# Kernel optimization log

Measured on AMD Instinct MI355X. Metric: run time of the kernel, lower is better.

Reference implementation:

```python
import jax, jax.numpy as jnp
import numpy as np

N_NODES = 100000
N_EDGES = 1_600_000
F_IN, HID, N_CLS = 128, 64, 32
NEG_SLOPE = 0.2  # PyG GATv2Conv default


def _segment_softmax(scores, seg, num_segments):
    # numerically stable softmax over edges grouped by destination node
    m = jax.ops.segment_max(scores, seg, num_segments=num_segments)
    ex = jnp.exp(scores - m[seg])
    s = jax.ops.segment_sum(ex, seg, num_segments=num_segments)
    return ex / (s[seg] + 1e-16)


def _gatv2_layer(x, src, dst, Wl, bl, Wr, br, att, bias, num_nodes):
    xl = x @ Wl + bl              # source transform  [N, C]
    xr = x @ Wr + br              # target transform  [N, C]
    # per-edge GATv2 attention logit: a . leaky_relu(xl_j + xr_i)
    e = jax.nn.leaky_relu(xl[src] + xr[dst], NEG_SLOPE) @ att  # [E]
    alpha = _segment_softmax(e, dst, num_nodes)                 # [E]
    out = jax.ops.segment_sum(alpha[:, None] * xl[src], dst, num_segments=num_nodes)
    return out + bias


def _add_self_loops(edge_index, n):
    loops = jnp.arange(n, dtype=edge_index.dtype)
    return jnp.concatenate([edge_index, jnp.stack([loops, loops])], axis=1)


def setup_inputs() -> dict:
    key = jax.random.key(0)
    ks = jax.random.split(key, 8)
    s1 = 1.0 / np.sqrt(F_IN)
    s2 = 1.0 / np.sqrt(HID)
    return {
        "x": jax.random.normal(ks[0], (N_NODES, F_IN), jnp.float32),
        "edge_index": jax.random.randint(ks[1], (2, N_EDGES), 0, N_NODES, jnp.int64),
        "W1l": jax.random.normal(ks[2], (F_IN, HID), jnp.float32) * s1,
        "b1l": jnp.zeros((HID,), jnp.float32),
        "W1r": jax.random.normal(ks[3], (F_IN, HID), jnp.float32) * s1,
        "b1r": jnp.zeros((HID,), jnp.float32),
        "att1": jax.random.normal(ks[4], (HID,), jnp.float32) * s2,
        "bias1": jnp.zeros((HID,), jnp.float32),
        "W2l": jax.random.normal(ks[5], (HID, N_CLS), jnp.float32) * s2,
        "b2l": jnp.zeros((N_CLS,), jnp.float32),
        "W2r": jax.random.normal(ks[6], (HID, N_CLS), jnp.float32) * s2,
        "b2r": jnp.zeros((N_CLS,), jnp.float32),
        "att2": jax.random.normal(ks[7], (N_CLS,), jnp.float32) / np.sqrt(N_CLS),
        "bias2": jnp.zeros((N_CLS,), jnp.float32),
    }


def reference(x, edge_index, W1l, b1l, W1r, b1r, att1, bias1,
              W2l, b2l, W2r, b2r, att2, bias2):
    n = x.shape[0]
    ei = _add_self_loops(edge_index, n)
    src, dst = ei[0], ei[1]
    h = jax.nn.relu(_gatv2_layer(x, src, dst, W1l, b1l, W1r, b1r, att1, bias1, n))
    # F.dropout(training=False) is identity in eval mode
    out = _gatv2_layer(h, src, dst, W2l, b2l, W2r, b2r, att2, bias2, n)
    return out
```

## Files before the change

### kernel.cpp

```cpp
#include <hip/hip_runtime.h>
#include <hip/hip_fp16.h>
#include <math.h>

#define F_IN 128
#define HID 64
#define NCLS 32
#define NEG 0.2f
#define NBKT 128
#define BSH 7
#define BMSK 127
#define CHUNK 4096

using bf8 = __attribute__((ext_vector_type(8))) short;
using f4v = __attribute__((ext_vector_type(4))) float;
typedef _Float16 hv2 __attribute__((ext_vector_type(2)));

__device__ __forceinline__ void f4fma(float4& a, float s, const float4& w) {
    a.x = fmaf(s, w.x, a.x);
    a.y = fmaf(s, w.y, a.y);
    a.z = fmaf(s, w.z, a.z);
    a.w = fmaf(s, w.w, a.w);
}
__device__ __forceinline__ unsigned short f2bf(float f) {
    unsigned u = __float_as_uint(f);
    return (unsigned short)((u + 0x7FFFu + ((u >> 16) & 1u)) >> 16);
}
__device__ __forceinline__ unsigned short f2h(float f) {
    return __half_as_ushort(__float2half(f));
}
__device__ __forceinline__ float h2f(unsigned short u) {
    return __half2float(__ushort_as_half(u));
}
__device__ __forceinline__ unsigned pkaddabs(unsigned a, unsigned b) {
    hv2 r = __builtin_bit_cast(hv2, a) + __builtin_bit_cast(hv2, b);
    return __builtin_bit_cast(unsigned, r) & 0x7FFF7FFFu;
}
__device__ __forceinline__ float fdot2(unsigned a, unsigned b, float c) {
    return __builtin_amdgcn_fdot2(__builtin_bit_cast(hv2, a),
                                  __builtin_bit_cast(hv2, b), c, false);
}
__device__ __forceinline__ float h2lo(unsigned a) {
    return (float)__builtin_bit_cast(hv2, a).x;
}
__device__ __forceinline__ float h2hi(unsigned a) {
    return (float)__builtin_bit_cast(hv2, a).y;
}
template <int CTRL>
__device__ __forceinline__ float dpp_add(float v) {
    int t = __builtin_amdgcn_update_dpp(0, __float_as_int(v), CTRL, 0xf, 0xf, true);
    return v + __int_as_float(t);
}


__global__ __launch_bounds__(256) void bucketHist(const int* __restrict__ ei,
                                                  int Eorig, int Etot,
                                                  int* __restrict__ bucketSize, int BK) {
    __shared__ int h[1024];
    int t = threadIdx.x;
    for (int j = t; j < BK; j += 256) h[j] = 0;
    __syncthreads();
    int base = blockIdx.x * CHUNK;
    int end = base + CHUNK < Etot ? base + CHUNK : Etot;
    for (int i = base + t; i < end; i += 256) {
        int dst = i < Eorig ? ei[Eorig + i] : i - Eorig;
        atomicAdd(&h[dst >> BSH], 1);
    }
    __syncthreads();
    for (int j = t; j < BK; j += 256)
        if (h[j]) atomicAdd(&bucketSize[j], h[j]);
}

__global__ __launch_bounds__(256) void bucketScan(const int* __restrict__ bucketSize,
                                                  int* __restrict__ bucketStart,
                                                  int* __restrict__ bucketCursor,
                                                  int BK, int Etot) {
    __shared__ int sd[256];
    int t = threadIdx.x;
    int v[4]; int ts = 0;
#pragma unroll
    for (int k = 0; k < 4; k++) {
        v[k] = (4 * t + k < BK) ? bucketSize[4 * t + k] : 0;
        ts += v[k];
    }
    sd[t] = ts;
    __syncthreads();
    for (int off = 1; off < 256; off <<= 1) {
        int x = (t >= off) ? sd[t - off] : 0;
        __syncthreads();
        sd[t] += x;
        __syncthreads();
    }
    int excl = sd[t] - ts;
#pragma unroll
    for (int k = 0; k < 4; k++) {
        if (4 * t + k < BK) { bucketStart[4 * t + k] = excl; bucketCursor[4 * t + k] = excl; }
        excl += v[k];
    }
    if (t == 255) bucketStart[BK] = Etot;
}

__global__ __launch_bounds__(256) void bucketScatter(const int* __restrict__ ei,
                                                     int Eorig, int Etot,
                                                     int* __restrict__ bucketCursor,
                                                     int* __restrict__ pairs, int BK) {
    __shared__ int h[1024], lbase[1024], hcur[1024];
    int t = threadIdx.x;
    for (int j = t; j < BK; j += 256) { h[j] = 0; hcur[j] = 0; }
    __syncthreads();
    int base = blockIdx.x * CHUNK;
    int end = base + CHUNK < Etot ? base + CHUNK : Etot;
    for (int i = base + t; i < end; i += 256) {
        int dst = i < Eorig ? ei[Eorig + i] : i - Eorig;
        atomicAdd(&h[dst >> BSH], 1);
    }
    __syncthreads();
    for (int j = t; j < BK; j += 256)
        lbase[j] = h[j] ? atomicAdd(&bucketCursor[j], h[j]) : 0;
    __syncthreads();
    for (int i = base + t; i < end; i += 256) {
        int src, dst;
        if (i < Eorig) { src = ei[i]; dst = ei[Eorig + i]; }
        else           { src = dst = i - Eorig; }
        int b = dst >> BSH;
        int off = atomicAdd(&hcur[b], 1);
        pairs[lbase[b] + off] = (src << BSH) | (dst & BMSK);
    }
}

__global__ __launch_bounds__(256) void bucketCSR(const int* __restrict__ pairs,
                                                 const int* __restrict__ bucketStart,
                                                 int* __restrict__ rowstart,
                                                 int* __restrict__ cnt,
                                                 int* __restrict__ srclist, int N) {
    __shared__ int c[256], cur[256];
    int t = threadIdx.x;
    int b = blockIdx.x;
    int lo = b * NBKT;
    int eb = bucketStart[b], ee = bucketStart[b + 1];
    c[t] = 0;
    __syncthreads();
    for (int i = eb + t; i < ee; i += 256)
        atomicAdd(&c[pairs[i] & BMSK], 1);
    __syncthreads();
    cur[t] = c[t];
    __syncthreads();
    for (int off = 1; off < 256; off <<= 1) {
        int x = (t >= off) ? cur[t - off] : 0;
        __syncthreads();
        cur[t] += x;
        __syncthreads();
    }
    int excl = cur[t] - c[t];
    int node = lo + t;
    if (t < NBKT && node < N) { rowstart[node] = eb + excl; cnt[node] = c[t]; }
    __syncthreads();
    cur[t] = excl;
    __syncthreads();
    for (int i = eb + t; i < ee; i += 256) {
        int v = pairs[i];
        int pos = atomicAdd(&cur[v & BMSK], 1);
        srclist[eb + pos] = v >> BSH;
    }
}

__global__ __launch_bounds__(256) void prepW(const float* __restrict__ Wl,
                                             const float* __restrict__ Wr,
                                             const float* __restrict__ att1,
                                             const float* __restrict__ att2,
                                             uint4* __restrict__ wfrag,
                                             unsigned short* __restrict__ att1h,
                                             unsigned short* __restrict__ att2h) {
    int e = blockIdx.x * 256 + threadIdx.x;
    if (e >= 2048) {
        int i = e - 2048;
        if (i < HID) att1h[i] = f2h(att1[i]);
        else if (i < HID + NCLS) att2h[i - HID] = f2h(att2[i - HID]);
        return;
    }
    int lane = e & 63;
    int kt = (e >> 6) & 3;
    int ct = (e >> 8) & 3;
    int mat = e >> 10;
    const float* W = mat ? Wr : Wl;
    int k0 = kt * 32 + (lane >> 4) * 8;
    int c = ct * 16 + (lane & 15);
    unsigned short h[8];
#pragma unroll
    for (int j = 0; j < 8; j++) h[j] = f2bf(W[(k0 + j) * HID + c]);
    wfrag[e] = *(uint4*)h;
}

__global__ __launch_bounds__(256) void transform1(const float* __restrict__ x,
                                                  const uint4* __restrict__ wfrag,
                                                  const float* __restrict__ bl,
                                                  const float* __restrict__ br,
                                                  const float* __restrict__ att,
                                                  unsigned short* __restrict__ xlh,
                                                  unsigned short* __restrict__ xrh,
                                                  float* __restrict__ sl, int N) {
    __shared__ uint4 sw[2048];
    int t = threadIdx.x;
#pragma unroll
    for (int j = 0; j < 8; j++) sw[t + j * 256] = wfrag[t + j * 256];
    __syncthreads();

    int w = t >> 6, lane = t & 63;
    int nb = blockIdx.x * 64 + w * 16;
    int m = lane & 15, quad = lane >> 4;

    int arow = nb + m; if (arow >= N) arow = N - 1;
    const float* xrow = x + (size_t)arow * F_IN + quad * 8;
    bf8 afr[4];
#pragma unroll
    for (int kt = 0; kt < 4; kt++) {
        float4 lo = *(const float4*)(xrow + kt * 32);
        float4 hi = *(const float4*)(xrow + kt * 32 + 4);
        unsigned short hh[8];
        hh[0] = f2bf(lo.x); hh[1] = f2bf(lo.y); hh[2] = f2bf(lo.z); hh[3] = f2bf(lo.w);
        hh[4] = f2bf(hi.x); hh[5] = f2bf(hi.y); hh[6] = f2bf(hi.z); hh[7] = f2bf(hi.w);
        afr[kt] = *(bf8*)hh;
    }

    float am[4];
#pragma unroll
    for (int ct = 0; ct < 4; ct++) am[ct] = att[ct * 16 + m];
    float slp[4] = {0.f, 0.f, 0.f, 0.f};

#pragma unroll
    for (int mat = 0; mat < 2; mat++) {
        const float* bias = mat ? br : bl;
#pragma unroll
        for (int ct = 0; ct < 4; ct++) {
            f4v acc = {0.f, 0.f, 0.f, 0.f};
#pragma unroll
            for (int kt = 0; kt < 4; kt++) {
                bf8 bfr = *(bf8*)&sw[((mat * 4 + ct) * 4 + kt) * 64 + lane];
                acc = __builtin_amdgcn_mfma_f32_16x16x32_bf16(afr[kt], bfr, acc, 0, 0, 0);
            }
            int ch = ct * 16 + m;
            float bv = bias[ch];
#pragma unroll
            for (int reg = 0; reg < 4; reg++) {
                int node = nb + quad * 4 + reg;
                float o = acc[reg] + bv;
                if (mat) {
                    if (node < N) xrh[(size_t)node * HID + ch] = f2h(o);
                } else {
                    unsigned short hb = f2h(o);
                    slp[reg] = fmaf(am[ct], h2f(hb), slp[reg]);
                    if (node < N) xlh[(size_t)node * HID + ch] = hb;
                }
            }
        }
    }
#pragma unroll
    for (int reg = 0; reg < 4; reg++) {
        slp[reg] = dpp_add<0xB1>(slp[reg]);
        slp[reg] = dpp_add<0x4E>(slp[reg]);
        slp[reg] = dpp_add<0x141>(slp[reg]);
        slp[reg] = dpp_add<0x140>(slp[reg]);
    }
    if (m == 0) {
#pragma unroll
        for (int reg = 0; reg < 4; reg++) {
            int node = nb + quad * 4 + reg;
            if (node < N) sl[node] = 0.6f * slp[reg];
        }
    }
}

__global__ __launch_bounds__(256) void transform2(const float* __restrict__ h,
                                                  const float* __restrict__ Wl,
                                                  const float* __restrict__ bl,
                                                  const float* __restrict__ Wr,
                                                  const float* __restrict__ br,
                                                  const float* __restrict__ att,
                                                  unsigned short* __restrict__ xlh,
                                                  unsigned short* __restrict__ xrh,
                                                  float* __restrict__ sl, int N) {
    __shared__ float sWl[HID * NCLS];
    __shared__ float sWr[HID * NCLS];
    __shared__ float sx[128][68];
    int t = threadIdx.x;
    int nb = blockIdx.x * 128;

#pragma unroll
    for (int j = 0; j < 2; j++) {
        int f = t + j * 256;
        ((float4*)sWl)[f] = ((const float4*)Wl)[f];
        ((float4*)sWr)[f] = ((const float4*)Wr)[f];
    }
    int maxf = (N - nb) * 16;
#pragma unroll
    for (int j = 0; j < 8; j++) {
        int f = t + j * 256;
        int node = f >> 4, kc = f & 15;
        float4 v = {0.f, 0.f, 0.f, 0.f};
        if (f < maxf) v = ((const float4*)(h + (size_t)nb * HID))[f];
        v.x = fmaxf(v.x, 0.f);
        v.y = fmaxf(v.y, 0.f);
        v.z = fmaxf(v.z, 0.f);
        v.w = fmaxf(v.w, 0.f);
        *(float4*)&sx[node][kc * 4] = v;
    }
    __syncthreads();

    int c4 = (t & 7) * 4;
    int slot = t >> 3;
    float4 bl4 = *(const float4*)(bl + c4);
    float4 br4 = *(const float4*)(br + c4);
    float4 at4 = *(const float4*)(att + c4);
    float4 accl[4] = {bl4, bl4, bl4, bl4};
    float4 accr[4] = {br4, br4, br4, br4};

#pragma unroll 4
    for (int k4 = 0; k4 < HID / 4; k4++) {
        int k = k4 * 4;
        float4 wl0 = *(const float4*)&sWl[(k + 0) * NCLS + c4];
        float4 wl1 = *(const float4*)&sWl[(k + 1) * NCLS + c4];
        float4 wl2 = *(const float4*)&sWl[(k + 2) * NCLS + c4];
        float4 wl3 = *(const float4*)&sWl[(k + 3) * NCLS + c4];
        float4 wr0 = *(const float4*)&sWr[(k + 0) * NCLS + c4];
        float4 wr1 = *(const float4*)&sWr[(k + 1) * NCLS + c4];
        float4 wr2 = *(const float4*)&sWr[(k + 2) * NCLS + c4];
        float4 wr3 = *(const float4*)&sWr[(k + 3) * NCLS + c4];
#pragma unroll
        for (int j = 0; j < 4; j++) {
            float4 xv = *(const float4*)&sx[slot + j * 32][k];
            f4fma(accl[j], xv.x, wl0); f4fma(accr[j], xv.x, wr0);
            f4fma(accl[j], xv.y, wl1); f4fma(accr[j], xv.y, wr1);
            f4fma(accl[j], xv.z, wl2); f4fma(accr[j], xv.z, wr2);
            f4fma(accl[j], xv.w, wl3); f4fma(accr[j], xv.w, wr3);
        }
    }
#pragma unroll
    for (int j = 0; j < 4; j++) {
        ushort4 o;
        o.x = f2h(accl[j].x); o.y = f2h(accl[j].y);
        o.z = f2h(accl[j].z); o.w = f2h(accl[j].w);
        ushort4 orr;
        orr.x = f2h(accr[j].x); orr.y = f2h(accr[j].y);
        orr.z = f2h(accr[j].z); orr.w = f2h(accr[j].w);
        float slpj = fmaf(at4.x, h2f(o.x),
                     fmaf(at4.y, h2f(o.y),
                     fmaf(at4.z, h2f(o.z), at4.w * h2f(o.w))));
        slpj = dpp_add<0xB1>(slpj);
        slpj = dpp_add<0x4E>(slpj);
        slpj = dpp_add<0x141>(slpj);
        int g = nb + slot + j * 32;
        if (g < N) {
            *(ushort4*)(xlh + (size_t)g * NCLS + c4) = o;
            *(ushort4*)(xrh + (size_t)g * NCLS + c4) = orr;
            if ((t & 7) == 0) sl[g] = 0.6f * slpj;
        }
    }
}

#define LOADROW(VP, SRC)                                                  \
    {                                                                     \
        const unsigned short* rp = xlh + (unsigned)(SRC) * C + cb0;       \
        if (NH == 4) *(uint4*)(VP) = *(const uint4*)rp;                   \
        else         *(uint2*)(VP) = *(const uint2*)rp;                   \
    }

#define COMPUTE(VP, T, B)                                                 \
    {                                                                     \
        float pa = 0.f;                                                   \
        _Pragma("unroll")                                                 \
        for (int j = 0; j < NH; j++)                                      \
            pa = fdot2(pkaddabs((VP)[j], xrp[j]), atp[j], pa);            \
        pa = dpp_add<0x128>(pa);                                          \
        pa += __shfl_xor(pa, 16, 64);                                     \
        pa += __shfl_xor(pa, 32, 64);                                     \
        float wgt = ((B) * 8 + slot < len) ? __expf(fmaf(0.4f, pa, (T)))  \
                                           : 0.f;                         \
        s += wgt;                                                         \
        _Pragma("unroll")                                                 \
        for (int j = 0; j < NH; j++) {                                    \
            acc[2 * j]     = fmaf(wgt, h2lo((VP)[j]), acc[2 * j]);        \
            acc[2 * j + 1] = fmaf(wgt, h2hi((VP)[j]), acc[2 * j + 1]);    \
        }                                                                 \
    }

template <int C>
__global__ __launch_bounds__(256) void fusedAggG(const unsigned short* __restrict__ xlh,
                                                 const unsigned short* __restrict__ xrh,
                                                 const unsigned short* __restrict__ atth,
                                                 const float* __restrict__ sl,
                                                 const int* __restrict__ rowstart,
                                                 const int* __restrict__ cnt,
                                                 const int* __restrict__ srclist,
                                                 const float* __restrict__ bias,
                                                 float* __restrict__ out, int N) {
    constexpr int CH = C / 8;
    constexpr int NH = CH / 2;
    int wid = threadIdx.x >> 6;
    int lane = threadIdx.x & 63;
    int n = blockIdx.x * 4 + wid;
    if (n >= N) return;

    int slot = lane & 7;
    int pos  = lane >> 3;
    int cb0  = pos * CH;

    unsigned xrp[NH], atp[NH];
    if (NH == 4) {
        *(uint4*)xrp = *(const uint4*)(xrh + (size_t)n * C + cb0);
        *(uint4*)atp = *(const uint4*)(atth + cb0);
    } else {
        *(uint2*)xrp = *(const uint2*)(xrh + (size_t)n * C + cb0);
        *(uint2*)atp = *(const uint2*)(atth + cb0);
    }

    int row = rowstart[n];
    int deg = cnt[n];

    float s = 0.f;
    float acc[CH];
#pragma unroll
    for (int c = 0; c < CH; c++) acc[c] = 0.f;

    for (int cb = 0; cb < deg; cb += 64) {
        int len = deg - cb; if (len > 64) len = 64;
        int len1 = len - 1;
        int li = lane < len ? lane : len1;
        int srcv = srclist[row + cb + li];
        float slv = sl[srcv];
        int nbatch = (len + 7) >> 3;

        float tA = __shfl(slv, slot, 64);
        int srcA = __shfl(srcv, slot, 64);
        unsigned vpA[NH], vpB[NH];
        float tB;
        LOADROW(vpA, srcA)

        int b = 0;
        while (true) {
            bool moreB = (b + 1 < nbatch);
            if (moreB) {
                int e = (b + 1) * 8 + slot;
                tB = __shfl(slv, e, 64);
                int srcB = __shfl(srcv, e, 64);
                LOADROW(vpB, srcB)
            }
            COMPUTE(vpA, tA, b)
            if (!moreB) break;
            bool moreA = (b + 2 < nbatch);
            if (moreA) {
                int e = (b + 2) * 8 + slot;
                tA = __shfl(slv, e, 64);
                int srcA2 = __shfl(srcv, e, 64);
                LOADROW(vpA, srcA2)
            }
            COMPUTE(vpB, tB, b + 1)
            if (!moreA) break;
            b += 2;
        }
    }
#pragma unroll
    for (int c = 0; c < CH; c++) {
        acc[c] = dpp_add<0xB1>(acc[c]);
        acc[c] = dpp_add<0x4E>(acc[c]);
        acc[c] = dpp_add<0x141>(acc[c]);
    }
    s = dpp_add<0xB1>(s);
    s = dpp_add<0x4E>(s);
    s = dpp_add<0x141>(s);

    if (slot == 0) {
        float inv = 1.f / (s + 1e-16f);
        float o8[CH];
        float bi[CH];
        if (NH == 4) {
            *(float4*)&bi[0] = *(const float4*)(bias + cb0);
            *(float4*)&bi[4] = *(const float4*)(bias + cb0 + 4);
        } else {
            *(float4*)&bi[0] = *(const float4*)(bias + cb0);
        }
#pragma unroll
        for (int c = 0; c < CH; c++) o8[c] = fmaf(acc[c], inv, bi[c]);
        if (NH == 4) {
            *(float4*)(out + (size_t)n * C + cb0)     = *(float4*)&o8[0];
            *(float4*)(out + (size_t)n * C + cb0 + 4) = *(float4*)&o8[4];
        } else {
            *(float4*)(out + (size_t)n * C + cb0) = *(float4*)&o8[0];
        }
    }
}

extern "C" void kernel_launch(void* const* d_in, const int* in_sizes, int n_in,
                              void* d_out, int out_size, void* d_ws, size_t ws_size,
                              hipStream_t stream) {
    const float* x     = (const float*)d_in[0];
    const int*   ei    = (const int*)d_in[1];
    const float* W1l   = (const float*)d_in[2];
    const float* b1l   = (const float*)d_in[3];
    const float* W1r   = (const float*)d_in[4];
    const float* b1r   = (const float*)d_in[5];
    const float* att1  = (const float*)d_in[6];
    const float* bias1 = (const float*)d_in[7];
    const float* W2l   = (const float*)d_in[8];
    const float* b2l   = (const float*)d_in[9];
    const float* W2r   = (const float*)d_in[10];
    const float* b2r   = (const float*)d_in[11];
    const float* att2  = (const float*)d_in[12];
    const float* bias2 = (const float*)d_in[13];
    float* out = (float*)d_out;

    int N     = in_sizes[0] / F_IN;
    int Eorig = in_sizes[1] / 2;
    int Etot  = Eorig + N;
    int BK    = (N + NBKT - 1) / NBKT;

    char* p = (char*)d_ws;
    auto alloc = [&](size_t bytes) { void* r = (void*)p; p += (bytes + 255) & ~(size_t)255; return r; };
    unsigned short* xl1h = (unsigned short*)alloc((size_t)N * HID * 2);
    unsigned short* xr1h = (unsigned short*)alloc((size_t)N * HID * 2);
    float* h       = (float*)alloc((size_t)N * HID * 4);
    unsigned short* xl2h = (unsigned short*)alloc((size_t)N * NCLS * 2);
    unsigned short* xr2h = (unsigned short*)alloc((size_t)N * NCLS * 2);
    int*   cnt     = (int*)alloc((size_t)N * 4);
    int*   rowstart= (int*)alloc((size_t)N * 4);
    int*   srclist = (int*)alloc((size_t)Etot * 4);
    uint4* wfrag   = (uint4*)alloc(2048 * 16);
    float* sl1     = (float*)alloc((size_t)N * 4);
    float* sl2     = (float*)alloc((size_t)N * 4);
    unsigned short* att1h = (unsigned short*)alloc(HID * 2);
    unsigned short* att2h = (unsigned short*)alloc(NCLS * 2);
    int*   bucketSize   = (int*)alloc(1040 * 4);
    int*   bucketStart  = (int*)alloc(1040 * 4);
    int*   bucketCursor = (int*)alloc(1040 * 4);
    int*   pairs   = (int*)h;

    int nChunks = (Etot + CHUNK - 1) / CHUNK;

    hipMemsetAsync(bucketSize, 0, 1040 * 4, stream);
    bucketHist<<<nChunks, 256, 0, stream>>>(ei, Eorig, Etot, bucketSize, BK);
    bucketScan<<<1, 256, 0, stream>>>(bucketSize, bucketStart, bucketCursor, BK, Etot);
    bucketScatter<<<nChunks, 256, 0, stream>>>(ei, Eorig, Etot, bucketCursor, pairs, BK);
    bucketCSR<<<BK, 256, 0, stream>>>(pairs, bucketStart, rowstart, cnt, srclist, N);

    prepW<<<9, 256, 0, stream>>>(W1l, W1r, att1, att2, wfrag, att1h, att2h);
    transform1<<<(N + 63) / 64, 256, 0, stream>>>(x, wfrag, b1l, b1r, att1, xl1h, xr1h, sl1, N);
    fusedAggG<HID><<<(N + 3) / 4, 256, 0, stream>>>(xl1h, xr1h, att1h, sl1, rowstart, cnt,
                                                    srclist, bias1, h, N);

    transform2<<<(N + 127) / 128, 256, 0, stream>>>(h, W2l, b2l, W2r, b2r, att2, xl2h, xr2h, sl2, N);
    fusedAggG<NCLS><<<(N + 3) / 4, 256, 0, stream>>>(xl2h, xr2h, att2h, sl2, rowstart, cnt,
                                                     srclist, bias2, out, N);
}
```

Baseline: 298.9 us.

## Store layer-1 output in fp16, fuse prepW into hist, two nodes per wave

Merges weight-fragment preparation into the histogram kernel as extra blocks, removing one launch. The intermediate hidden activations are written as fp16 instead of fp32, which halves the write in aggregation 1 and the read in transform2. The aggregation kernel now handles two nodes per wave across a loop, halving the grid size. fp16 storage of h adds rounding error, and the per-wave loop may cut parallelism or latency hiding.

```diff
diff --git a/kernel.cpp b/kernel.cpp
--- a/kernel.cpp
+++ b/kernel.cpp
@@ -52,11 +52,51 @@
 }
 
 
-__global__ __launch_bounds__(256) void bucketHist(const int* __restrict__ ei,
-                                                  int Eorig, int Etot,
-                                                  int* __restrict__ bucketSize, int BK) {
+__device__ __forceinline__ void prepW_body(int pb, int t,
+                                           const float* __restrict__ Wl,
+                                           const float* __restrict__ Wr,
+                                           const float* __restrict__ att1,
+                                           const float* __restrict__ att2,
+                                           uint4* __restrict__ wfrag,
+                                           unsigned short* __restrict__ att1h,
+                                           unsigned short* __restrict__ att2h) {
+    int e = pb * 256 + t;
+    if (e >= 2048) {
+        int i = e - 2048;
+        if (i < HID) att1h[i] = f2h(att1[i]);
+        else if (i < HID + NCLS) att2h[i - HID] = f2h(att2[i - HID]);
+        return;
+    }
+    int lane = e & 63;
+    int kt = (e >> 6) & 3;
+    int ct = (e >> 8) & 3;
+    int mat = e >> 10;
+    const float* W = mat ? Wr : Wl;
+    int k0 = kt * 32 + (lane >> 4) * 8;
+    int c = ct * 16 + (lane & 15);
+    unsigned short h[8];
+#pragma unroll
+    for (int j = 0; j < 8; j++) h[j] = f2bf(W[(k0 + j) * HID + c]);
+    wfrag[e] = *(uint4*)h;
+}
+
+__global__ __launch_bounds__(256) void histPrep(const int* __restrict__ ei,
+                                                int Eorig, int Etot,
+                                                int* __restrict__ bucketSize, int BK,
+                                                int nChunks,
+                                                const float* __restrict__ Wl,
+                                                const float* __restrict__ Wr,
+                                                const float* __restrict__ att1,
+                                                const float* __restrict__ att2,
+                                                uint4* __restrict__ wfrag,
+                                                unsigned short* __restrict__ att1h,
+                                                unsigned short* __restrict__ att2h) {
     __shared__ int h[1024];
     int t = threadIdx.x;
+    if ((int)blockIdx.x >= nChunks) {
+        prepW_body(blockIdx.x - nChunks, t, Wl, Wr, att1, att2, wfrag, att1h, att2h);
+        return;
+    }
     for (int j = t; j < BK; j += 256) h[j] = 0;
     __syncthreads();
     int base = blockIdx.x * CHUNK;
@@ -163,33 +203,6 @@
     }
 }
 
-__global__ __launch_bounds__(256) void prepW(const float* __restrict__ Wl,
-                                             const float* __restrict__ Wr,
-                                             const float* __restrict__ att1,
-                                             const float* __restrict__ att2,
-                                             uint4* __restrict__ wfrag,
-                                             unsigned short* __restrict__ att1h,
-                                             unsigned short* __restrict__ att2h) {
-    int e = blockIdx.x * 256 + threadIdx.x;
-    if (e >= 2048) {
-        int i = e - 2048;
-        if (i < HID) att1h[i] = f2h(att1[i]);
-        else if (i < HID + NCLS) att2h[i - HID] = f2h(att2[i - HID]);
-        return;
-    }
-    int lane = e & 63;
-    int kt = (e >> 6) & 3;
-    int ct = (e >> 8) & 3;
-    int mat = e >> 10;
-    const float* W = mat ? Wr : Wl;
-    int k0 = kt * 32 + (lane >> 4) * 8;
-    int c = ct * 16 + (lane & 15);
-    unsigned short h[8];
-#pragma unroll
-    for (int j = 0; j < 8; j++) h[j] = f2bf(W[(k0 + j) * HID + c]);
-    wfrag[e] = *(uint4*)h;
-}
-
 __global__ __launch_bounds__(256) void transform1(const float* __restrict__ x,
                                                   const uint4* __restrict__ wfrag,
                                                   const float* __restrict__ bl,
@@ -269,7 +282,7 @@
     }
 }
 
-__global__ __launch_bounds__(256) void transform2(const float* __restrict__ h,
+__global__ __launch_bounds__(256) void transform2(const unsigned short* __restrict__ hh,
                                                   const float* __restrict__ Wl,
                                                   const float* __restrict__ bl,
                                                   const float* __restrict__ Wr,
@@ -290,18 +303,20 @@
         ((float4*)sWl)[f] = ((const float4*)Wl)[f];
         ((float4*)sWr)[f] = ((const float4*)Wr)[f];
     }
-    int maxf = (N - nb) * 16;
-#pragma unroll
-    for (int j = 0; j < 8; j++) {
+    int maxf = (N - nb) * 8;
+#pragma unroll
+    for (int j = 0; j < 4; j++) {
         int f = t + j * 256;
-        int node = f >> 4, kc = f & 15;
-        float4 v = {0.f, 0.f, 0.f, 0.f};
-        if (f < maxf) v = ((const float4*)(h + (size_t)nb * HID))[f];
-        v.x = fmaxf(v.x, 0.f);
-        v.y = fmaxf(v.y, 0.f);
-        v.z = fmaxf(v.z, 0.f);
-        v.w = fmaxf(v.w, 0.f);
-        *(float4*)&sx[node][kc * 4] = v;
+        int node = f >> 3, kc = f & 7;
+        uint4 q = {0u, 0u, 0u, 0u};
+        if (f < maxf) q = ((const uint4*)(hh + (size_t)nb * HID))[f];
+        float4 a, b4;
+        a.x = fmaxf(h2lo(q.x), 0.f); a.y = fmaxf(h2hi(q.x), 0.f);
+        a.z = fmaxf(h2lo(q.y), 0.f); a.w = fmaxf(h2hi(q.y), 0.f);
+        b4.x = fmaxf(h2lo(q.z), 0.f); b4.y = fmaxf(h2hi(q.z), 0.f);
+        b4.z = fmaxf(h2lo(q.w), 0.f); b4.w = fmaxf(h2hi(q.w), 0.f);
+        *(float4*)&sx[node][kc * 8]     = a;
+        *(float4*)&sx[node][kc * 8 + 4] = b4;
     }
     __syncthreads();
 
@@ -382,7 +397,7 @@
         }                                                                 \
     }
 
-template <int C>
+template <int C, bool HOUT>
 __global__ __launch_bounds__(256) void fusedAggG(const unsigned short* __restrict__ xlh,
                                                  const unsigned short* __restrict__ xrh,
                                                  const unsigned short* __restrict__ atth,
@@ -391,99 +406,112 @@
                                                  const int* __restrict__ cnt,
                                                  const int* __restrict__ srclist,
                                                  const float* __restrict__ bias,
-                                                 float* __restrict__ out, int N) {
+                                                 void* __restrict__ outp, int N) {
     constexpr int CH = C / 8;
     constexpr int NH = CH / 2;
     int wid = threadIdx.x >> 6;
     int lane = threadIdx.x & 63;
-    int n = blockIdx.x * 4 + wid;
-    if (n >= N) return;
 
     int slot = lane & 7;
     int pos  = lane >> 3;
     int cb0  = pos * CH;
 
-    unsigned xrp[NH], atp[NH];
-    if (NH == 4) {
-        *(uint4*)xrp = *(const uint4*)(xrh + (size_t)n * C + cb0);
-        *(uint4*)atp = *(const uint4*)(atth + cb0);
-    } else {
-        *(uint2*)xrp = *(const uint2*)(xrh + (size_t)n * C + cb0);
-        *(uint2*)atp = *(const uint2*)(atth + cb0);
-    }
-
-    int row = rowstart[n];
-    int deg = cnt[n];
-
-    float s = 0.f;
-    float acc[CH];
-#pragma unroll
-    for (int c = 0; c < CH; c++) acc[c] = 0.f;
-
-    for (int cb = 0; cb < deg; cb += 64) {
-        int len = deg - cb; if (len > 64) len = 64;
-        int len1 = len - 1;
-        int li = lane < len ? lane : len1;
-        int srcv = srclist[row + cb + li];
-        float slv = sl[srcv];
-        int nbatch = (len + 7) >> 3;
-
-        float tA = __shfl(slv, slot, 64);
-        int srcA = __shfl(srcv, slot, 64);
-        unsigned vpA[NH], vpB[NH];
-        float tB;
-        LOADROW(vpA, srcA)
-
-        int b = 0;
-        while (true) {
-            bool moreB = (b + 1 < nbatch);
-            if (moreB) {
-                int e = (b + 1) * 8 + slot;
-                tB = __shfl(slv, e, 64);
-                int srcB = __shfl(srcv, e, 64);
-                LOADROW(vpB, srcB)
+    for (int rep = 0; rep < 2; rep++) {
+        int n = blockIdx.x * 8 + rep * 4 + wid;
+        if (n >= N) break;
+
+        unsigned xrp[NH], atp[NH];
+        if (NH == 4) {
+            *(uint4*)xrp = *(const uint4*)(xrh + (size_t)n * C + cb0);
+            *(uint4*)atp = *(const uint4*)(atth + cb0);
+        } else {
+            *(uint2*)xrp = *(const uint2*)(xrh + (size_t)n * C + cb0);
+            *(uint2*)atp = *(const uint2*)(atth + cb0);
+        }
+
+        int row = rowstart[n];
+        int deg = cnt[n];
+
+        float s = 0.f;
+        float acc[CH];
+#pragma unroll
+        for (int c = 0; c < CH; c++) acc[c] = 0.f;
+
+        for (int cb = 0; cb < deg; cb += 64) {
+            int len = deg - cb; if (len > 64) len = 64;
+            int len1 = len - 1;
+            int li = lane < len ? lane : len1;
+            int srcv = srclist[row + cb + li];
+            float slv = sl[srcv];
+            int nbatch = (len + 7) >> 3;
+
+            float tA = __shfl(slv, slot, 64);
+            int srcA = __shfl(srcv, slot, 64);
+            unsigned vpA[NH], vpB[NH];
+            float tB;
+            LOADROW(vpA, srcA)
+
+            int b = 0;
+            while (true) {
+                bool moreB = (b + 1 < nbatch);
+                if (moreB) {
+                    int e = (b + 1) * 8 + slot;
+                    tB = __shfl(slv, e, 64);
+                    int srcB = __shfl(srcv, e, 64);
+                    LOADROW(vpB, srcB)
+                }
+                COMPUTE(vpA, tA, b)
+                if (!moreB) break;
+                bool moreA = (b + 2 < nbatch);
+                if (moreA) {
+                    int e = (b + 2) * 8 + slot;
+                    tA = __shfl(slv, e, 64);
+                    int srcA2 = __shfl(srcv, e, 64);
+                    LOADROW(vpA, srcA2)
+                }
+                COMPUTE(vpB, tB, b + 1)
+                if (!moreA) break;
+                b += 2;
             }
-            COMPUTE(vpA, tA, b)
-            if (!moreB) break;
-            bool moreA = (b + 2 < nbatch);
-            if (moreA) {
-                int e = (b + 2) * 8 + slot;
-                tA = __shfl(slv, e, 64);
-                int srcA2 = __shfl(srcv, e, 64);
-                LOADROW(vpA, srcA2)
+        }
+#pragma unroll
+        for (int c = 0; c < CH; c++) {
+            acc[c] = dpp_add<0xB1>(acc[c]);
+            acc[c] = dpp_add<0x4E>(acc[c]);
+            acc[c] = dpp_add<0x141>(acc[c]);
+        }
+        s = dpp_add<0xB1>(s);
+        s = dpp_add<0x4E>(s);
+        s = dpp_add<0x141>(s);
+
+        if (slot == 0) {
+            float inv = 1.f / (s + 1e-16f);
+            float o8[CH];
+            float bi[CH];
+            if (NH == 4) {
+                *(float4*)&bi[0] = *(const float4*)(bias + cb0);
+                *(float4*)&bi[4] = *(const float4*)(bias + cb0 + 4);
+            } else {
+                *(float4*)&bi[0] = *(const float4*)(bias + cb0);
             }
-            COMPUTE(vpB, tB, b + 1)
-            if (!moreA) break;
-            b += 2;
-        }
-    }
-#pragma unroll
-    for (int c = 0; c < CH; c++) {
-        acc[c] = dpp_add<0xB1>(acc[c]);
-        acc[c] = dpp_add<0x4E>(acc[c]);
-        acc[c] = dpp_add<0x141>(acc[c]);
-    }
-    s = dpp_add<0xB1>(s);
-    s = dpp_add<0x4E>(s);
-    s = dpp_add<0x141>(s);
-
-    if (slot == 0) {
-        float inv = 1.f / (s + 1e-16f);
-        float o8[CH];
-        float bi[CH];
-        if (NH == 4) {
-            *(float4*)&bi[0] = *(const float4*)(bias + cb0);
-            *(float4*)&bi[4] = *(const float4*)(bias + cb0 + 4);
-        } else {
-            *(float4*)&bi[0] = *(const float4*)(bias + cb0);
-        }
-#pragma unroll
-        for (int c = 0; c < CH; c++) o8[c] = fmaf(acc[c], inv, bi[c]);
-        if (NH == 4) {
-            *(float4*)(out + (size_t)n * C + cb0)     = *(float4*)&o8[0];
-            *(float4*)(out + (size_t)n * C + cb0 + 4) = *(float4*)&o8[4];
-        } else {
-            *(float4*)(out + (size_t)n * C + cb0) = *(float4*)&o8[0];
+#pragma unroll
+            for (int c = 0; c < CH; c++) o8[c] = fmaf(acc[c], inv, bi[c]);
+            if (HOUT) {
+                unsigned short oh[CH];
+#pragma unroll
+                for (int c = 0; c < CH; c++) oh[c] = f2h(o8[c]);
+                unsigned short* op = (unsigned short*)outp + (size_t)n * C + cb0;
+                if (NH == 4) *(uint4*)op = *(uint4*)oh;
+                else         *(uint2*)op = *(uint2*)oh;
+            } else {
+                float* op = (float*)outp + (size_t)n * C + cb0;
+                if (NH == 4) {
+                    *(float4*)op       = *(float4*)&o8[0];
+                    *(float4*)(op + 4) = *(float4*)&o8[4];
+                } else {
+                    *(float4*)op = *(float4*)&o8[0];
+                }
+            }
         }
     }
 }
@@ -516,7 +544,7 @@
     auto alloc = [&](size_t bytes) { void* r = (void*)p; p += (bytes + 255) & ~(size_t)255; return r; };
     unsigned short* xl1h = (unsigned short*)alloc((size_t)N * HID * 2);
     unsigned short* xr1h = (unsigned short*)alloc((size_t)N * HID * 2);
-    float* h       = (float*)alloc((size_t)N * HID * 4);
+    unsigned short* h    = (unsigned short*)alloc((size_t)N * HID * 2);
     unsigned short* xl2h = (unsigned short*)alloc((size_t)N * NCLS * 2);
     unsigned short* xr2h = (unsigned short*)alloc((size_t)N * NCLS * 2);
     int*   cnt     = (int*)alloc((size_t)N * 4);
@@ -535,17 +563,17 @@
     int nChunks = (Etot + CHUNK - 1) / CHUNK;
 
     hipMemsetAsync(bucketSize, 0, 1040 * 4, stream);
-    bucketHist<<<nChunks, 256, 0, stream>>>(ei, Eorig, Etot, bucketSize, BK);
+    histPrep<<<nChunks + 9, 256, 0, stream>>>(ei, Eorig, Etot, bucketSize, BK, nChunks,
+                                              W1l, W1r, att1, att2, wfrag, att1h, att2h);
     bucketScan<<<1, 256, 0, stream>>>(bucketSize, bucketStart, bucketCursor, BK, Etot);
     bucketScatter<<<nChunks, 256, 0, stream>>>(ei, Eorig, Etot, bucketCursor, pairs, BK);
     bucketCSR<<<BK, 256, 0, stream>>>(pairs, bucketStart, rowstart, cnt, srclist, N);
 
-    prepW<<<9, 256, 0, stream>>>(W1l, W1r, att1, att2, wfrag, att1h, att2h);
     transform1<<<(N + 63) / 64, 256, 0, stream>>>(x, wfrag, b1l, b1r, att1, xl1h, xr1h, sl1, N);
-    fusedAggG<HID><<<(N + 3) / 4, 256, 0, stream>>>(xl1h, xr1h, att1h, sl1, rowstart, cnt,
-                                                    srclist, bias1, h, N);
+    fusedAggG<HID, true><<<(N + 7) / 8, 256, 0, stream>>>(xl1h, xr1h, att1h, sl1, rowstart, cnt,
+                                                          srclist, bias1, h, N);
 
     transform2<<<(N + 127) / 128, 256, 0, stream>>>(h, W2l, b2l, W2r, b2r, att2, xl2h, xr2h, sl2, N);
-    fusedAggG<NCLS><<<(N + 3) / 4, 256, 0, stream>>>(xl2h, xr2h, att2h, sl2, rowstart, cnt,
-                                                     srclist, bias2, out, N);
-}
+    fusedAggG<NCLS, false><<<(N + 7) / 8, 256, 0, stream>>>(xl2h, xr2h, att2h, sl2, rowstart, cnt,
+                                                            srclist, bias2, out, N);
+}
```

Measured after the change: 292.0 us. -2.3%, faster.
